# Kernel optimization log

Measured on AMD Instinct MI355X. Metric: run time of the kernel, lower is better.

## Reference

```python
import jax, jax.numpy as jnp
import numpy as np

NUM_HEADS = 8
NUM_GROUPS = 32
EPS = 1e-5


def group_norm(x, gamma, beta):
    B, C, H, W = x.shape
    xg = x.reshape(B, NUM_GROUPS, C // NUM_GROUPS * H * W)
    mean = xg.mean(axis=-1, keepdims=True)
    var = xg.var(axis=-1, keepdims=True)
    xg = (xg - mean) * jax.lax.rsqrt(var + EPS)
    xn = xg.reshape(B, C, H, W)
    return xn * gamma[None, :, None, None] + beta[None, :, None, None]


def setup_inputs() -> dict:
    key = jax.random.key(0)
    ks = jax.random.split(key, 7)
    C = 512
    B, H, W = 8, 32, 32
    x = jax.random.normal(ks[0], (B, C, H, W), dtype=jnp.float32)
    gamma = jnp.ones((C,), dtype=jnp.float32)
    beta = jnp.zeros((C,), dtype=jnp.float32)
    # 1x1 conv weights stored as [out, in]
    w_qkv = jax.random.normal(ks[1], (3 * C, C), dtype=jnp.float32) * (1.0 / np.sqrt(C))
    b_qkv = jax.random.normal(ks[2], (3 * C,), dtype=jnp.float32) * 0.02
    w_proj = jax.random.normal(ks[3], (C, C), dtype=jnp.float32) * (1.0 / np.sqrt(C))
    b_proj = jax.random.normal(ks[4], (C,), dtype=jnp.float32) * 0.02
    return {"x": x, "gamma": gamma, "beta": beta, "w_qkv": w_qkv,
            "b_qkv": b_qkv, "w_proj": w_proj, "b_proj": b_proj}


def reference(x, gamma, beta, w_qkv, b_qkv, w_proj, b_proj):
    B, C, H, W = x.shape
    hd = C // NUM_HEADS  # head_dim
    x_norm = group_norm(x, gamma, beta)
    # 1x1 conv: [B,C,H,W] x [3C,C] -> [B,3C,H,W]
    qkv = jnp.einsum('bchw,oc->bohw', x_norm, w_qkv) + b_qkv[None, :, None, None]
    q, k, v = jnp.split(qkv, 3, axis=1)
    N = H * W
    q = q.reshape(B, NUM_HEADS, hd, N)
    k = k.reshape(B, NUM_HEADS, hd, N)
    v = v.reshape(B, NUM_HEADS, hd, N)
    attn = jnp.einsum('bhcn,bhcm->bhnm', q, k) * (hd ** -0.5)
    attn = jax.nn.softmax(attn, axis=-1)
    out = jnp.einsum('bhnm,bhcm->bhcn', attn, v)
    out = out.reshape(B, C, H, W)
    proj = jnp.einsum('bchw,oc->bohw', out, w_proj) + b_proj[None, :, None, None]
    return x + proj
```

## Files before the change

kernel.cpp:

```cpp
#include <hip/hip_runtime.h>
#include <hip/hip_bf16.h>

#define BB 8
#define CC 512
#define NN 1024
#define NG 32
#define CPG 16
#define NH 8
#define HD 64
#define C3 1536
#define QKLD 1024

typedef __hip_bfloat16 bf16;
typedef unsigned short ushort_t;

typedef __attribute__((ext_vector_type(8))) short bf16x8;
typedef __attribute__((ext_vector_type(8))) unsigned short ushortx8;
typedef __attribute__((ext_vector_type(4))) float floatx4;

__device__ __forceinline__ float b2f(bf16 h) { return __bfloat162float(h); }
__device__ __forceinline__ bf16 f2b(float f) { return __float2bfloat16(f); }
__device__ __forceinline__ ushort_t f2us(float f) {
    bf16 h = __float2bfloat16(f);
    return *(ushort_t*)&h;
}

#define GLD16(gsrc, ldst)                                                        \
    __builtin_amdgcn_global_load_lds(                                            \
        (const __attribute__((address_space(1))) unsigned int*)(const void*)(gsrc), \
        (__attribute__((address_space(3))) unsigned int*)(void*)(ldst), 16, 0, 0)

__global__ __launch_bounds__(1024, 1) void gn_kernel(const float* __restrict__ x,
                                                     const float* __restrict__ gamma,
                                                     const float* __restrict__ beta,
                                                     bf16* __restrict__ xnT,
                                                     const float* __restrict__ wqkv,
                                                     const float* __restrict__ wproj,
                                                     ushort_t* __restrict__ wqkvB,
                                                     ushort_t* __restrict__ wprojB) {
    int tid = threadIdx.x;
    if (blockIdx.x >= 256) {
        int wb = blockIdx.x - 256;
        const float* src;
        ushort_t* dst;
        int base;
        if (wb < 192) { src = wqkv; dst = wqkvB; base = wb * 4096; }
        else          { src = wproj; dst = wprojB; base = (wb - 192) * 4096; }
        int o = base + tid * 4;
        float4 f = *(const float4*)(src + o);
        ushort_t u[4] = {f2us(f.x), f2us(f.y), f2us(f.z), f2us(f.w)};
        *(uint2*)(dst + o) = *(uint2*)u;
        return;
    }

    const int GSZ = CPG * NN;
    int b = blockIdx.x >> 5;
    int g = blockIdx.x & 31;
    size_t base = ((size_t)b * CC + (size_t)g * CPG) * NN;

    int c_loc = tid >> 6;
    int nsp   = (tid & 63) * 16;
    const float* srcp = x + base + (size_t)c_loc * NN + nsp;

    float fv[16];
    *(float4*)(fv + 0)  = *(const float4*)(srcp + 0);
    *(float4*)(fv + 4)  = *(const float4*)(srcp + 4);
    *(float4*)(fv + 8)  = *(const float4*)(srcp + 8);
    *(float4*)(fv + 12) = *(const float4*)(srcp + 12);
    float s = 0.f, s2 = 0.f;
#pragma unroll
    for (int j = 0; j < 16; ++j) { float v = fv[j]; s += v; s2 += v * v; }

#pragma unroll
    for (int off = 32; off > 0; off >>= 1) {
        s  += __shfl_down(s, off, 64);
        s2 += __shfl_down(s2, off, 64);
    }
    __shared__ float rs[16], rs2[16], stat[2];
    __shared__ ushort_t Lt[16][1032];
    int wid = tid >> 6, lane = tid & 63;
    if (lane == 0) { rs[wid] = s; rs2[wid] = s2; }
    __syncthreads();
    if (tid == 0) {
        float ts = 0.f, ts2 = 0.f;
#pragma unroll
        for (int w = 0; w < 16; ++w) { ts += rs[w]; ts2 += rs2[w]; }
        float mean = ts * (1.f / GSZ);
        float var  = ts2 * (1.f / GSZ) - mean * mean;
        stat[0] = mean;
        stat[1] = rsqrtf(var + 1e-5f);
    }
    __syncthreads();
    float mean = stat[0], inv = stat[1];

    float ga = gamma[g * CPG + c_loc];
    float be = beta[g * CPG + c_loc];

    ushortx8 u0, u1;
#pragma unroll
    for (int j = 0; j < 8; ++j) {
        u0[j] = f2us((fv[j]     - mean) * inv * ga + be);
        u1[j] = f2us((fv[j + 8] - mean) * inv * ga + be);
    }
    *(ushortx8*)&Lt[c_loc][nsp]     = u0;
    *(ushortx8*)&Lt[c_loc][nsp + 8] = u1;
    __syncthreads();

    ushort_t o16[16];
#pragma unroll
    for (int c = 0; c < 16; ++c) o16[c] = Lt[c][tid];
    ushort_t* dst = (ushort_t*)xnT + ((size_t)b * NN + tid) * CC + g * CPG;
    *(uint4*)dst       = *(const uint4*)(o16);
    *(uint4*)(dst + 8) = *(const uint4*)(o16 + 8);
}

__global__ __launch_bounds__(256) void qkv_gemm(const ushort_t* __restrict__ wB,
                                                const bf16* __restrict__ xnT,
                                                const float* __restrict__ bias,
                                                bf16* __restrict__ qkT,
                                                bf16* __restrict__ vN) {
    __shared__ ushort_t Wl[128 * 64];
    __shared__ ushort_t Xl[128 * 64];
    int b  = blockIdx.z;
    int o0 = blockIdx.y * 128;
    int n0 = blockIdx.x * 128;
    int tid = threadIdx.x;
    int wv = tid >> 6, l = tid & 63, ln = l & 15, qd = (l >> 4) & 3;
    int wm = wv >> 1, wn = wv & 1;

    int strow = wv * 32 + (l >> 3);
    int sgran = (l & 7) ^ (l >> 3);
    const ushort_t* wsrc = wB + (size_t)(o0 + strow) * CC + sgran * 8;
    const ushort_t* xsrc = (const ushort_t*)xnT + ((size_t)b * NN + n0 + strow) * CC + sgran * 8;

    floatx4 acc[4][4];
#pragma unroll
    for (int i = 0; i < 4; ++i)
#pragma unroll
        for (int j = 0; j < 4; ++j) acc[i][j] = (floatx4){0.f, 0.f, 0.f, 0.f};

    for (int k0 = 0; k0 < CC; k0 += 64) {
#pragma unroll
        for (int c = 0; c < 4; ++c) {
            GLD16(wsrc + k0 + (size_t)c * 8 * CC, &Wl[(wv * 32 + c * 8) * 64]);
            GLD16(xsrc + k0 + (size_t)c * 8 * CC, &Xl[(wv * 32 + c * 8) * 64]);
        }
        __syncthreads();
#pragma unroll
        for (int kk = 0; kk < 2; ++kk) {
            int qs = ((kk * 4 + qd) ^ (ln & 7)) * 8;
            bf16x8 af[4], bfr[4];
#pragma unroll
            for (int i = 0; i < 4; ++i)
                af[i] = *(const bf16x8*)&Wl[(wm * 64 + i * 16 + ln) * 64 + qs];
#pragma unroll
            for (int j = 0; j < 4; ++j)
                bfr[j] = *(const bf16x8*)&Xl[(wn * 64 + j * 16 + ln) * 64 + qs];
#pragma unroll
            for (int i = 0; i < 4; ++i)
#pragma unroll
                for (int j = 0; j < 4; ++j)
                    acc[i][j] = __builtin_amdgcn_mfma_f32_16x16x32_bf16(af[i], bfr[j], acc[i][j], 0, 0, 0);
        }
        __syncthreads();
    }

    if (o0 < 1024) {
#pragma unroll
        for (int i = 0; i < 4; ++i) {
            int ob = o0 + wm * 64 + i * 16 + qd * 4;
            float sc = (ob < 512) ? 0.18033688011112042f : 1.0f;
#pragma unroll
            for (int j = 0; j < 4; ++j) {
                int n = n0 + wn * 64 + j * 16 + ln;
                ushort_t pk[4];
#pragma unroll
                for (int r = 0; r < 4; ++r)
                    pk[r] = f2us((acc[i][j][r] + bias[ob + r]) * sc);
                *(uint2*)((ushort_t*)qkT + ((size_t)b * NN + n) * QKLD + ob) = *(uint2*)pk;
            }
        }
    } else {
#pragma unroll
        for (int i = 0; i < 4; ++i) {
#pragma unroll
            for (int r = 0; r < 4; ++r) {
                int o = o0 + wm * 64 + i * 16 + qd * 4 + r;
                float bb = bias[o];
                size_t rb = ((size_t)b * CC + (o - 1024)) * NN + n0 + wn * 64 + ln;
#pragma unroll
                for (int j = 0; j < 4; ++j)
                    vN[rb + j * 16] = f2b(acc[i][j][r] + bb);
            }
        }
    }
}

__global__ __launch_bounds__(256, 4) void attn_kernel(const bf16* __restrict__ qkTp,
                                                      const bf16* __restrict__ vNp,
                                                      bf16* __restrict__ aoT) {
    __shared__ ushort_t Kt[2][64 * 64];
    __shared__ ushort_t Vn[2][64 * 64];
    __shared__ ushort_t Pw[4][16 * 64];

    int h  = blockIdx.x;
    int qt = blockIdx.y;
    int bi = blockIdx.z;
    int q0 = qt * 64;
    int tid = threadIdx.x;
    int wq = tid >> 6;
    int l  = tid & 63;
    int ln = l & 15;
    int qd = (l >> 4) & 3;
    int l7 = ln & 7;
    int lb = ln >> 3;

    const ushort_t* qkT = (const ushort_t*)qkTp;
    const ushort_t* vN  = (const ushort_t*)vNp;

    const ushort_t* qsrc = qkT + ((size_t)bi * NN + q0 + wq * 16 + ln) * QKLD + h * HD + qd * 8;
    bf16x8 aq0 = *(const bf16x8*)(qsrc);
    bf16x8 aq1 = *(const bf16x8*)(qsrc + 32);

    bf16x8 ones;
#pragma unroll
    for (int j = 0; j < 8; ++j) ones[j] = (short)0x3F80;

    floatx4 O[4];
#pragma unroll
    for (int t = 0; t < 4; ++t) O[t] = (floatx4){0.f, 0.f, 0.f, 0.f};
    floatx4 lsum = (floatx4){0.f, 0.f, 0.f, 0.f};

    ushort_t* Pme = &Pw[wq][0];

    int ksl0 = (qd ^ l7) * 8;
    int ksl1 = ((qd + 4) ^ l7) * 8;

    int srow = tid >> 2;
    int g1   = tid & 3;
    int s7   = srow & 7;
    int ko1  = (g1 ^ s7) * 8;
    int ko2  = ((g1 + 4) ^ s7) * 8;
    const ushort_t* ks = qkT + ((size_t)bi * NN + srow) * QKLD + 512 + h * HD + g1 * 8;
    const ushort_t* vs = vN + ((size_t)bi * CC + h * HD + srow) * NN + g1 * 8;

    uint4 kr0 = *(const uint4*)(ks);
    uint4 kr1 = *(const uint4*)(ks + 32);
    uint4 vr0 = *(const uint4*)(vs);
    uint4 vr1 = *(const uint4*)(vs + 32);
    {
        ushort_t* kd = &Kt[0][srow * 64];
        *(uint4*)(kd + ko1) = kr0; *(uint4*)(kd + ko2) = kr1;
        ushort_t* vd = &Vn[0][srow * 64];
        *(uint4*)(vd + ko1) = vr0; *(uint4*)(vd + ko2) = vr1;
    }
    kr0 = *(const uint4*)(ks + (size_t)64 * QKLD);
    kr1 = *(const uint4*)(ks + (size_t)64 * QKLD + 32);
    vr0 = *(const uint4*)(vs + 64);
    vr1 = *(const uint4*)(vs + 64 + 32);
    __syncthreads();

    for (int it = 0; it < 16; ++it) {
        int cur = it & 1;
        const ushort_t* KtC = &Kt[cur][0];
        const ushort_t* VnC = &Vn[cur][0];
        if (it < 15) {
            ushort_t* kd = &Kt[cur ^ 1][srow * 64];
            *(uint4*)(kd + ko1) = kr0; *(uint4*)(kd + ko2) = kr1;
            ushort_t* vd = &Vn[cur ^ 1][srow * 64];
            *(uint4*)(vd + ko1) = vr0; *(uint4*)(vd + ko2) = vr1;
        }
        if (it < 14) {
            size_t mo = (size_t)(it + 2) * 64;
            kr0 = *(const uint4*)(ks + mo * QKLD);
            kr1 = *(const uint4*)(ks + mo * QKLD + 32);
            vr0 = *(const uint4*)(vs + mo);
            vr1 = *(const uint4*)(vs + mo + 32);
        }

        floatx4 S[4];
#pragma unroll
        for (int t = 0; t < 4; ++t) {
            const ushort_t* krow = KtC + (t * 16 + ln) * 64;
            bf16x8 b0 = *(const bf16x8*)(krow + ksl0);
            bf16x8 b1 = *(const bf16x8*)(krow + ksl1);
            floatx4 acc = (floatx4){0.f, 0.f, 0.f, 0.f};
            acc = __builtin_amdgcn_mfma_f32_16x16x32_bf16(aq0, b0, acc, 0, 0, 0);
            acc = __builtin_amdgcn_mfma_f32_16x16x32_bf16(aq1, b1, acc, 0, 0, 0);
            S[t] = acc;
        }

#pragma unroll
        for (int t = 0; t < 4; ++t) {
#pragma unroll
            for (int r = 0; r < 4; ++r) {
                float p = exp2f(S[t][r]);
                int qr = qd * 4 + r;
                Pme[qr * 64 + ((t * 2 + lb) ^ (qr & 7)) * 8 + l7] = f2us(p);
            }
        }
        bf16x8 pa0 = *(const bf16x8*)&Pme[ln * 64 + ksl0];
        bf16x8 pa1 = *(const bf16x8*)&Pme[ln * 64 + ksl1];

        lsum = __builtin_amdgcn_mfma_f32_16x16x32_bf16(pa0, ones, lsum, 0, 0, 0);
        lsum = __builtin_amdgcn_mfma_f32_16x16x32_bf16(pa1, ones, lsum, 0, 0, 0);

#pragma unroll
        for (int t = 0; t < 4; ++t) {
            const ushort_t* vrow = VnC + (t * 16 + ln) * 64;
            bf16x8 v0 = *(const bf16x8*)(vrow + ksl0);
            bf16x8 v1 = *(const bf16x8*)(vrow + ksl1);
            O[t] = __builtin_amdgcn_mfma_f32_16x16x32_bf16(pa0, v0, O[t], 0, 0, 0);
            O[t] = __builtin_amdgcn_mfma_f32_16x16x32_bf16(pa1, v1, O[t], 0, 0, 0);
        }
        if (it < 15) __syncthreads();
    }

    float inv[4];
#pragma unroll
    for (int r = 0; r < 4; ++r) inv[r] = 1.f / lsum[r];
#pragma unroll
    for (int t = 0; t < 4; ++t) {
#pragma unroll
        for (int r = 0; r < 4; ++r) {
            int n = q0 + wq * 16 + qd * 4 + r;
            ((ushort_t*)aoT)[((size_t)bi * NN + n) * CC + h * HD + t * 16 + ln] =
                f2us(O[t][r] * inv[r]);
        }
    }
}

__global__ __launch_bounds__(256) void proj_gemm(const bf16* __restrict__ aoT,
                                                 const ushort_t* __restrict__ wB,
                                                 const float* __restrict__ bias,
                                                 const float* __restrict__ xres,
                                                 float* __restrict__ out) {
    __shared__ ushort_t Wl[64 * 64];
    __shared__ ushort_t Xl[64 * 64];
    int b  = blockIdx.z;
    int o0 = blockIdx.y * 64;
    int n0 = blockIdx.x * 64;
    int tid = threadIdx.x;
    int wv = tid >> 6, l = tid & 63, ln = l & 15, qd = (l >> 4) & 3;
    int wm = wv >> 1, wn = wv & 1;

    int strow = wv * 16 + (l >> 3);
    int sgran = (l & 7) ^ (l >> 3);
    const ushort_t* xsrc = (const ushort_t*)aoT + ((size_t)b * NN + n0 + strow) * CC + sgran * 8;
    const ushort_t* wsrc = wB + (size_t)(o0 + strow) * CC + sgran * 8;

    floatx4 acc[2][2];
#pragma unroll
    for (int i = 0; i < 2; ++i)
#pragma unroll
        for (int j = 0; j < 2; ++j) acc[i][j] = (floatx4){0.f, 0.f, 0.f, 0.f};

    for (int k0 = 0; k0 < CC; k0 += 64) {
#pragma unroll
        for (int c = 0; c < 2; ++c) {
            GLD16(wsrc + k0 + (size_t)c * 8 * CC, &Wl[(wv * 16 + c * 8) * 64]);
            GLD16(xsrc + k0 + (size_t)c * 8 * CC, &Xl[(wv * 16 + c * 8) * 64]);
        }
        __syncthreads();
#pragma unroll
        for (int kk = 0; kk < 2; ++kk) {
            int qs = ((kk * 4 + qd) ^ (ln & 7)) * 8;
            bf16x8 af[2], bfr[2];
#pragma unroll
            for (int i = 0; i < 2; ++i)
                af[i] = *(const bf16x8*)&Wl[(wm * 32 + i * 16 + ln) * 64 + qs];
#pragma unroll
            for (int j = 0; j < 2; ++j)
                bfr[j] = *(const bf16x8*)&Xl[(wn * 32 + j * 16 + ln) * 64 + qs];
#pragma unroll
            for (int i = 0; i < 2; ++i)
#pragma unroll
                for (int j = 0; j < 2; ++j)
                    acc[i][j] = __builtin_amdgcn_mfma_f32_16x16x32_bf16(af[i], bfr[j], acc[i][j], 0, 0, 0);
        }
        __syncthreads();
    }

#pragma unroll
    for (int i = 0; i < 2; ++i) {
#pragma unroll
        for (int r = 0; r < 4; ++r) {
            int o = o0 + wm * 32 + i * 16 + qd * 4 + r;
            float bb = bias[o];
            size_t rb = ((size_t)b * CC + o) * NN + n0 + wn * 32 + ln;
#pragma unroll
            for (int j = 0; j < 2; ++j)
                out[rb + j * 16] = acc[i][j][r] + bb + xres[rb + j * 16];
        }
    }
}

extern "C" void kernel_launch(void* const* d_in, const int* in_sizes, int n_in,
                              void* d_out, int out_size, void* d_ws, size_t ws_size,
                              hipStream_t stream) {
    const float* x      = (const float*)d_in[0];
    const float* gamma  = (const float*)d_in[1];
    const float* beta   = (const float*)d_in[2];
    const float* w_qkv  = (const float*)d_in[3];
    const float* b_qkv  = (const float*)d_in[4];
    const float* w_proj = (const float*)d_in[5];
    const float* b_proj = (const float*)d_in[6];
    float* out = (float*)d_out;

    bf16* xnT = (bf16*)d_ws;
    bf16* qkT = xnT + (size_t)BB * CC * NN;
    bf16* vN  = qkT + (size_t)BB * NN * QKLD;
    ushort_t* wqkvB  = (ushort_t*)(vN + (size_t)BB * CC * NN);
    ushort_t* wprojB = wqkvB + (size_t)C3 * CC;
    bf16* aoT = xnT;

    gn_kernel<<<512, 1024, 0, stream>>>(x, gamma, beta, xnT,
                                        w_qkv, w_proj, wqkvB, wprojB);
    qkv_gemm<<<dim3(NN / 128, C3 / 128, BB), 256, 0, stream>>>(wqkvB, xnT, b_qkv, qkT, vN);
    attn_kernel<<<dim3(NH, NN / 64, BB), 256, 0, stream>>>(qkT, vN, aoT);
    proj_gemm<<<dim3(NN / 64, CC / 64, BB), 256, 0, stream>>>(aoT, wprojB, b_proj, x, out);
}
```

Measured before the change: 154.8 us.

## Double-buffer QKV GEMM shared-memory tiles with async prefetch of next K slices

Restructures the qkv_gemm main loop to use two 32-wide K-slice shared-memory buffers instead of a single 64-wide buffer. Global-to-LDS loads for slice kt+2 are issued while MFMAs run on slice kt, with explicit vmcnt waits and barriers replacing the full syncthreads pair. This is meant to hide global load latency behind compute, at the cost of more loop iterations, more barriers, and a narrower 4-granule XOR swizzle.

```diff
diff --git a/kernel.cpp b/kernel.cpp
--- a/kernel.cpp
+++ b/kernel.cpp
@@ -119,8 +119,8 @@
                                                 const float* __restrict__ bias,
                                                 bf16* __restrict__ qkT,
                                                 bf16* __restrict__ vN) {
-    __shared__ ushort_t Wl[128 * 64];
-    __shared__ ushort_t Xl[128 * 64];
+    __shared__ ushort_t Wl[2][128 * 32];
+    __shared__ ushort_t Xl[2][128 * 32];
     int b  = blockIdx.z;
     int o0 = blockIdx.y * 128;
     int n0 = blockIdx.x * 128;
@@ -128,10 +128,21 @@
     int wv = tid >> 6, l = tid & 63, ln = l & 15, qd = (l >> 4) & 3;
     int wm = wv >> 1, wn = wv & 1;
 
-    int strow = wv * 32 + (l >> 3);
-    int sgran = (l & 7) ^ (l >> 3);
+    int strow = wv * 32 + (l >> 2);
+    int sgran = (l & 3) ^ ((l >> 2) & 3);
     const ushort_t* wsrc = wB + (size_t)(o0 + strow) * CC + sgran * 8;
     const ushort_t* xsrc = (const ushort_t*)xnT + ((size_t)b * NN + n0 + strow) * CC + sgran * 8;
+    int lr0 = (wv * 32) * 32;
+    int lr1 = (wv * 32 + 16) * 32;
+
+#define QKV_STAGE(t, bf)                                         \
+    do {                                                         \
+        int ko_ = (t) * 32;                                      \
+        GLD16(wsrc + ko_, &Wl[bf][lr0]);                         \
+        GLD16(wsrc + ko_ + 16 * CC, &Wl[bf][lr1]);               \
+        GLD16(xsrc + ko_, &Xl[bf][lr0]);                         \
+        GLD16(xsrc + ko_ + 16 * CC, &Xl[bf][lr1]);               \
+    } while (0)
 
     floatx4 acc[4][4];
 #pragma unroll
@@ -139,31 +150,32 @@
 #pragma unroll
         for (int j = 0; j < 4; ++j) acc[i][j] = (floatx4){0.f, 0.f, 0.f, 0.f};
 
-    for (int k0 = 0; k0 < CC; k0 += 64) {
-#pragma unroll
-        for (int c = 0; c < 4; ++c) {
-            GLD16(wsrc + k0 + (size_t)c * 8 * CC, &Wl[(wv * 32 + c * 8) * 64]);
-            GLD16(xsrc + k0 + (size_t)c * 8 * CC, &Xl[(wv * 32 + c * 8) * 64]);
-        }
-        __syncthreads();
-#pragma unroll
-        for (int kk = 0; kk < 2; ++kk) {
-            int qs = ((kk * 4 + qd) ^ (ln & 7)) * 8;
-            bf16x8 af[4], bfr[4];
-#pragma unroll
-            for (int i = 0; i < 4; ++i)
-                af[i] = *(const bf16x8*)&Wl[(wm * 64 + i * 16 + ln) * 64 + qs];
+    int qs = (qd ^ (ln & 3)) * 8;
+
+    QKV_STAGE(0, 0);
+    QKV_STAGE(1, 1);
+
+    for (int kt = 0; kt < 16; ++kt) {
+        if (kt < 15) { asm volatile("s_waitcnt vmcnt(4)" ::: "memory"); }
+        else         { asm volatile("s_waitcnt vmcnt(0)" ::: "memory"); }
+        __builtin_amdgcn_s_barrier();
+        int cb = kt & 1;
+        bf16x8 af[4], bfr[4];
+#pragma unroll
+        for (int i = 0; i < 4; ++i)
+            af[i] = *(const bf16x8*)&Wl[cb][(wm * 64 + i * 16 + ln) * 32 + qs];
+#pragma unroll
+        for (int j = 0; j < 4; ++j)
+            bfr[j] = *(const bf16x8*)&Xl[cb][(wn * 64 + j * 16 + ln) * 32 + qs];
+#pragma unroll
+        for (int i = 0; i < 4; ++i)
 #pragma unroll
             for (int j = 0; j < 4; ++j)
-                bfr[j] = *(const bf16x8*)&Xl[(wn * 64 + j * 16 + ln) * 64 + qs];
-#pragma unroll
-            for (int i = 0; i < 4; ++i)
-#pragma unroll
-                for (int j = 0; j < 4; ++j)
-                    acc[i][j] = __builtin_amdgcn_mfma_f32_16x16x32_bf16(af[i], bfr[j], acc[i][j], 0, 0, 0);
-        }
-        __syncthreads();
-    }
+                acc[i][j] = __builtin_amdgcn_mfma_f32_16x16x32_bf16(af[i], bfr[j], acc[i][j], 0, 0, 0);
+        __builtin_amdgcn_s_barrier();
+        if (kt + 2 < 16) QKV_STAGE(kt + 2, cb);
+    }
+#undef QKV_STAGE
 
     if (o0 < 1024) {
 #pragma unroll
```

After: 154.7 us. Within noise of the previous version (-0.1%).
